# Kernel tuning notes

Hardware: AMD Instinct MI355X
Metric: run time of the kernel (lower is better)

The kernel has to match this reference:

```python
import jax, jax.numpy as jnp
import numpy as np

N, E = 100000, 1600000
IN_C, HID, OUT_C, EDGE_D, GRAPH_D = 32, 32, 8, 16, 16

def _lin_w(key, fan_in, fan_out):
    return jax.random.normal(key, (fan_in, fan_out), dtype=jnp.float32) * (1.0 / np.sqrt(fan_in))

def setup_inputs() -> dict:
    key = jax.random.key(0)
    ks = jax.random.split(key, 12)
    return {
        "x": jax.random.uniform(ks[0], (N, IN_C), dtype=jnp.float32),
        "edge_attr": jax.random.uniform(ks[1], (E, EDGE_D), dtype=jnp.float32),
        "graph_attr": jax.random.uniform(ks[2], (1, GRAPH_D), dtype=jnp.float32),
        "edge_index": jax.random.randint(ks[3], (2, E), 0, N, dtype=jnp.int32),
        "batch": jnp.zeros((N,), dtype=jnp.int32),
        "W_node": _lin_w(ks[4], IN_C, HID),
        "b_node": jnp.zeros((HID,), jnp.float32),
        "W_graph": _lin_w(ks[5], GRAPH_D, GRAPH_D),
        "b_graph": jnp.zeros((GRAPH_D,), jnp.float32),
        "W_edge_agg": _lin_w(ks[6], 2 * HID + EDGE_D + GRAPH_D, EDGE_D),
        "b_edge_agg": jnp.zeros((EDGE_D,), jnp.float32),
        "W_node_agg": _lin_w(ks[7], EDGE_D + HID + GRAPH_D, HID),
        "b_node_agg": jnp.zeros((HID,), jnp.float32),
        "W_sage_l": _lin_w(ks[8], HID, OUT_C),
        "b_sage_l": jnp.zeros((OUT_C,), jnp.float32),
        "W_sage_r": _lin_w(ks[9], HID, OUT_C),
    }

def _seg_mean(vals, idx, num_segments):
    # scatter-mean: sum per segment / count (count clamped to 1 for empty segments)
    sums = jax.ops.segment_sum(vals, idx, num_segments=num_segments)
    cnt = jax.ops.segment_sum(jnp.ones((vals.shape[0],), vals.dtype), idx, num_segments=num_segments)
    return sums / jnp.maximum(cnt, 1.0)[:, None]

def reference(x, edge_attr, graph_attr, edge_index, batch,
              W_node, b_node, W_graph, b_graph,
              W_edge_agg, b_edge_agg, W_node_agg, b_node_agg,
              W_sage_l, b_sage_l, W_sage_r):
    n = x.shape[0]
    row, col = edge_index[0], edge_index[1]
    # node / graph embeddings (plain linear, no activation)
    h_i = x @ W_node + b_node                       # [N, HID]
    h_G = graph_attr @ W_graph + b_graph            # [1, GRAPH_D]
    h_G_e = jnp.broadcast_to(h_G, (row.shape[0], h_G.shape[1]))
    # edge aggregator: gather both endpoints, concat, linear, relu
    edge_in = jnp.concatenate([h_i[row], h_i[col], edge_attr, h_G_e], axis=-1)  # [E, 96]
    h_edge_agg = jax.nn.relu(edge_in @ W_edge_agg + b_edge_agg)                 # [E, EDGE_D]
    # per-node mean of edges whose source == node (replaces O(N*E) python loop)
    m_N = _seg_mean(h_edge_agg, row, n)             # [N, EDGE_D]
    # node aggregator
    h_G_n = jnp.broadcast_to(h_G, (n, h_G.shape[1]))
    h_i2 = jax.nn.relu(jnp.concatenate([h_i, m_N, h_G_n], axis=-1) @ W_node_agg + b_node_agg)
    # SAGEConv (mean aggr): out = lin_l(mean_{j->i} x_j) + lin_r(x_i)
    agg = _seg_mean(h_i2[row], col, n)
    h_nodes = agg @ W_sage_l + b_sage_l + h_i2 @ W_sage_r  # [N, OUT_C]
    # global mean pool over batch assignment (single graph here)
    pooled = _seg_mean(h_nodes, batch, 1)           # [1, OUT_C]
    return jax.nn.log_softmax(pooled, axis=1)
```

## Files before the change

kernel.cpp:

```cpp
#include <hip/hip_runtime.h>
#include <hip/hip_fp16.h>

#define HID 32
#define IN_C 32
#define EDGE_D 16
#define GRAPH_D 16
#define OUT_C 8
#define STRIDE 48

__global__ void __launch_bounds__(256)
k_node_emb(const float* __restrict__ x,
           const float* __restrict__ W,
           const float* __restrict__ b,
           const float* __restrict__ graph_attr,
           const float* __restrict__ W_graph,
           const float* __restrict__ b_graph,
           const float* __restrict__ W_edge_agg,
           const float* __restrict__ b_edge_agg,
           const float* __restrict__ W_node_agg,
           const float* __restrict__ b_node_agg,
           float* __restrict__ bias_edge,
           float* __restrict__ bias_node,
           int* __restrict__ zero_base, int zero_count,
           __half* __restrict__ h, int n) {
    __shared__ float hG[GRAPH_D];
    int t = threadIdx.x;
    for (int idx = blockIdx.x * blockDim.x + t; idx < zero_count;
         idx += gridDim.x * blockDim.x)
        zero_base[idx] = 0;

    if (blockIdx.x == 0 && t < GRAPH_D) {
        float acc = b_graph[t];
        for (int d = 0; d < GRAPH_D; d++)
            acc += graph_attr[d] * W_graph[d * GRAPH_D + t];
        hG[t] = acc;
    }
    __syncthreads();
    if (blockIdx.x == 0) {
        if (t < EDGE_D) {
            float acc = b_edge_agg[t];
            for (int d = 0; d < GRAPH_D; d++)
                acc += hG[d] * W_edge_agg[(2 * HID + EDGE_D + d) * EDGE_D + t];
            bias_edge[t] = acc;
        }
        if (t < HID) {
            float acc = b_node_agg[t];
            for (int d = 0; d < GRAPH_D; d++)
                acc += hG[d] * W_node_agg[(HID + EDGE_D + d) * HID + t];
            bias_node[t] = acc;
        }
    }

    int i = blockIdx.x * blockDim.x + t;
    if (i >= n) return;
    float in[IN_C];
    const float4* xr = (const float4*)(x + (size_t)i * IN_C);
#pragma unroll
    for (int q = 0; q < IN_C / 4; q++) {
        float4 v = xr[q];
        in[4 * q + 0] = v.x; in[4 * q + 1] = v.y;
        in[4 * q + 2] = v.z; in[4 * q + 3] = v.w;
    }
    float acc[HID];
#pragma unroll
    for (int j = 0; j < HID; j++) acc[j] = b[j];
#pragma unroll
    for (int k = 0; k < IN_C; k++) {
        float a = in[k];
#pragma unroll
        for (int j = 0; j < HID; j++) acc[j] += a * W[k * HID + j];
    }
    float4 packed[4];
    __half2* ph = (__half2*)packed;
#pragma unroll
    for (int j = 0; j < 16; j++)
        ph[j] = __floats2half2_rn(acc[2 * j], acc[2 * j + 1]);
    float4* hr = (float4*)(h + (size_t)i * HID);
#pragma unroll
    for (int q = 0; q < 4; q++) hr[q] = packed[q];
}

__global__ void __launch_bounds__(256)
k_edge_place(const int* __restrict__ ei,
             const __half* __restrict__ hi,
             const float* __restrict__ ea,
             const float* __restrict__ We,
             const float* __restrict__ biasE,
             int* __restrict__ cur_row,
             int* __restrict__ cur_col,
             __half* __restrict__ he_bucket, int E) {
    int e = blockIdx.x * blockDim.x + threadIdx.x;
    if (e >= E) return;
    int r = ei[e];
    int c = ei[E + e];
    int pr = atomicAdd(cur_row + r, 1);
    atomicAdd(cur_col + c, 1);

    float in[80];
    {
        float4 t[4];
        const float4* hr4 = (const float4*)(hi + (size_t)r * HID);
#pragma unroll
        for (int q = 0; q < 4; q++) t[q] = hr4[q];
        const __half2* hp = (const __half2*)t;
#pragma unroll
        for (int j = 0; j < 16; j++) {
            float2 f = __half22float2(hp[j]);
            in[2 * j] = f.x; in[2 * j + 1] = f.y;
        }
    }
    {
        float4 t[4];
        const float4* hc4 = (const float4*)(hi + (size_t)c * HID);
#pragma unroll
        for (int q = 0; q < 4; q++) t[q] = hc4[q];
        const __half2* hp = (const __half2*)t;
#pragma unroll
        for (int j = 0; j < 16; j++) {
            float2 f = __half22float2(hp[j]);
            in[32 + 2 * j] = f.x; in[32 + 2 * j + 1] = f.y;
        }
    }
    {
        const float4* er = (const float4*)(ea + (size_t)e * EDGE_D);
#pragma unroll
        for (int q = 0; q < 4; q++) {
            float4 v = er[q];
            in[64 + 4 * q + 0] = v.x; in[64 + 4 * q + 1] = v.y;
            in[64 + 4 * q + 2] = v.z; in[64 + 4 * q + 3] = v.w;
        }
    }
    float acc[EDGE_D];
#pragma unroll
    for (int j = 0; j < EDGE_D; j++) acc[j] = biasE[j];
#pragma unroll
    for (int k = 0; k < 80; k++) {
        float a = in[k];
#pragma unroll
        for (int j = 0; j < EDGE_D; j++) acc[j] += a * We[k * EDGE_D + j];
    }

    if (pr < STRIDE) {
        float4 packed[2];
        __half2* ph = (__half2*)packed;
#pragma unroll
        for (int j = 0; j < 8; j++)
            ph[j] = __floats2half2_rn(fmaxf(acc[2 * j], 0.f),
                                      fmaxf(acc[2 * j + 1], 0.f));
        float4* dst = (float4*)(he_bucket + ((size_t)r * STRIDE + pr) * EDGE_D);
        dst[0] = packed[0];
        dst[1] = packed[1];
    }
}

#define RNODES 128
__global__ void __launch_bounds__(256)
k_reduce(const __half* __restrict__ hi,
         const __half* __restrict__ he_bucket,
         const int* __restrict__ cur_row,
         const int* __restrict__ batch,
         const float* __restrict__ Wna,
         const float* __restrict__ Wsl,
         const float* __restrict__ Wsr,
         const float* __restrict__ biasN,
         __half* __restrict__ zout,
         float* __restrict__ pool,
         float* __restrict__ ncnt, int n) {
    __shared__ float ms_s[RNODES][EDGE_D + 1];
    __shared__ int cnt_s[RNODES];
    __shared__ float red[4][OUT_C + 1];
    __shared__ float redc[4];
    int tid = threadIdx.x;
    int g = tid >> 4;
    int l = tid & 15;
    int base = blockIdx.x * RNODES;

    if (tid < RNODES)
        cnt_s[tid] = (base + tid < n) ? cur_row[base + tid] : 0;
    __syncthreads();

    for (int iter = 0; iter < RNODES / 16; iter++) {
        int node = base + iter * 16 + g;
        int cnt = cnt_s[iter * 16 + g];
        int d = cnt < STRIDE ? cnt : STRIDE;
        float inv = 1.0f / fmaxf((float)cnt, 1.0f);
        float a16[EDGE_D];
#pragma unroll
        for (int j = 0; j < EDGE_D; j++) a16[j] = 0.f;
        const __half* bb = he_bucket + (size_t)node * STRIDE * EDGE_D;
        for (int t = l; t < d; t += 16) {
            const float4* rp = (const float4*)(bb + t * EDGE_D);
            float4 lo = rp[0], hi4 = rp[1];
            const __half2* hp0 = (const __half2*)&lo;
            const __half2* hp1 = (const __half2*)&hi4;
#pragma unroll
            for (int j = 0; j < 4; j++) {
                float2 f0 = __half22float2(hp0[j]);
                float2 f1 = __half22float2(hp1[j]);
                a16[2 * j]     += f0.x; a16[2 * j + 1] += f0.y;
                a16[8 + 2 * j] += f1.x; a16[8 + 2 * j + 1] += f1.y;
            }
        }
#pragma unroll
        for (int m = 8; m >= 1; m >>= 1) {
#pragma unroll
            for (int k = 0; k < m; k++) {
                float send = (l & m) ? a16[k] : a16[k + m];
                float recv = __shfl_xor(send, m, 16);
                float keep = (l & m) ? a16[k + m] : a16[k];
                a16[k] = keep + recv;
            }
        }
        ms_s[iter * 16 + g][l] = a16[0] * inv;
    }
    __syncthreads();

    int i = base + tid;
    float rvv[OUT_C];
#pragma unroll
    for (int j = 0; j < OUT_C; j++) rvv[j] = 0.f;
    float cc = 0.f;

    if (tid < RNODES && i < n) {
        float ms[EDGE_D];
#pragma unroll
        for (int k = 0; k < EDGE_D; k++) ms[k] = ms_s[tid][k];

        float hr[HID];
        {
            float4 t[4];
            const float4* hrow = (const float4*)(hi + (size_t)i * HID);
#pragma unroll
            for (int q = 0; q < 4; q++) t[q] = hrow[q];
            const __half2* hp = (const __half2*)t;
#pragma unroll
            for (int j = 0; j < 16; j++) {
                float2 f = __half22float2(hp[j]);
                hr[2 * j] = f.x; hr[2 * j + 1] = f.y;
            }
        }
        float h2[HID];
#pragma unroll
        for (int j = 0; j < HID; j++) h2[j] = biasN[j];
#pragma unroll
        for (int k = 0; k < HID; k++) {
            float a = hr[k];
#pragma unroll
            for (int j = 0; j < HID; j++) h2[j] += a * Wna[k * HID + j];
        }
#pragma unroll
        for (int k = 0; k < EDGE_D; k++) {
            float a = ms[k];
#pragma unroll
            for (int j = 0; j < HID; j++) h2[j] += a * Wna[(HID + k) * HID + j];
        }
#pragma unroll
        for (int j = 0; j < HID; j++) h2[j] = fmaxf(h2[j], 0.f);

        float zv[OUT_C];
#pragma unroll
        for (int j = 0; j < OUT_C; j++) zv[j] = 0.f;
#pragma unroll
        for (int k = 0; k < HID; k++) {
            float a = h2[k];
#pragma unroll
            for (int j = 0; j < OUT_C; j++) {
                zv[j]  += a * Wsl[k * OUT_C + j];
                rvv[j] += a * Wsr[k * OUT_C + j];
            }
        }
        float4 packed;
        __half2* ph = (__half2*)&packed;
#pragma unroll
        for (int j = 0; j < 4; j++)
            ph[j] = __floats2half2_rn(zv[2 * j], zv[2 * j + 1]);
        *(float4*)(zout + (size_t)i * OUT_C) = packed;
        if (batch[i] == 0) cc = 1.f; else {
#pragma unroll
            for (int j = 0; j < OUT_C; j++) rvv[j] = 0.f;
        }
    }
#pragma unroll
    for (int off = 32; off > 0; off >>= 1) {
#pragma unroll
        for (int j = 0; j < OUT_C; j++) rvv[j] += __shfl_down(rvv[j], off, 64);
        cc += __shfl_down(cc, off, 64);
    }
    int w = tid >> 6;
    if ((tid & 63) == 0) {
#pragma unroll
        for (int j = 0; j < OUT_C; j++) red[w][j] = rvv[j];
        redc[w] = cc;
    }
    __syncthreads();
    if (tid < OUT_C) {
        float s = red[0][tid] + red[1][tid] + red[2][tid] + red[3][tid];
        atomicAdd(pool + tid, s);
    }
    if (tid == OUT_C) {
        atomicAdd(ncnt, redc[0] + redc[1] + redc[2] + redc[3]);
    }
}

#define POOL_BLOCKS 1280
__global__ void __launch_bounds__(256)
k_pool(const int* __restrict__ ei,
       const __half* __restrict__ z,
       const int* __restrict__ cur_col,
       float* __restrict__ pool, int E) {
    __shared__ float red[4][OUT_C + 1];
    int tid = threadIdx.x;
    float w8[OUT_C];
#pragma unroll
    for (int j = 0; j < OUT_C; j++) w8[j] = 0.f;
    for (int e = blockIdx.x * blockDim.x + tid; e < E;
         e += gridDim.x * blockDim.x) {
        int r = ei[e];
        int c = ei[E + e];
        float inv = 1.0f / fmaxf((float)cur_col[c], 1.0f);
        float4 t = *(const float4*)(z + (size_t)r * OUT_C);
        const __half2* hp = (const __half2*)&t;
#pragma unroll
        for (int j = 0; j < 4; j++) {
            float2 f = __half22float2(hp[j]);
            w8[2 * j]     += f.x * inv;
            w8[2 * j + 1] += f.y * inv;
        }
    }
#pragma unroll
    for (int off = 32; off > 0; off >>= 1) {
#pragma unroll
        for (int j = 0; j < OUT_C; j++) w8[j] += __shfl_down(w8[j], off, 64);
    }
    int w = tid >> 6;
    if ((tid & 63) == 0) {
#pragma unroll
        for (int j = 0; j < OUT_C; j++) red[w][j] = w8[j];
    }
    __syncthreads();
    if (tid < OUT_C) {
        float s = red[0][tid] + red[1][tid] + red[2][tid] + red[3][tid];
        atomicAdd(pool + tid, s);
    }
}

__global__ void k_final(const float* __restrict__ pool,
                        const float* __restrict__ ncnt,
                        const float* __restrict__ bsl,
                        float* __restrict__ out) {
    if (threadIdx.x == 0 && blockIdx.x == 0) {
        float c = fmaxf(ncnt[0], 1.0f);
        float p[OUT_C];
        float m = -1e30f;
#pragma unroll
        for (int j = 0; j < OUT_C; j++) {
            p[j] = pool[j] / c + bsl[j];
            m = fmaxf(m, p[j]);
        }
        float s = 0.f;
#pragma unroll
        for (int j = 0; j < OUT_C; j++) s += expf(p[j] - m);
        float l = logf(s);
#pragma unroll
        for (int j = 0; j < OUT_C; j++) out[j] = p[j] - m - l;
    }
}

extern "C" void kernel_launch(void* const* d_in, const int* in_sizes, int n_in,
                              void* d_out, int out_size, void* d_ws, size_t ws_size,
                              hipStream_t stream) {
    const float* x          = (const float*)d_in[0];
    const float* edge_attr  = (const float*)d_in[1];
    const float* graph_attr = (const float*)d_in[2];
    const int*   edge_index = (const int*)d_in[3];
    const int*   batch      = (const int*)d_in[4];
    const float* W_node     = (const float*)d_in[5];
    const float* b_node     = (const float*)d_in[6];
    const float* W_graph    = (const float*)d_in[7];
    const float* b_graph    = (const float*)d_in[8];
    const float* W_edge_agg = (const float*)d_in[9];
    const float* b_edge_agg = (const float*)d_in[10];
    const float* W_node_agg = (const float*)d_in[11];
    const float* b_node_agg = (const float*)d_in[12];
    const float* W_sage_l   = (const float*)d_in[13];
    const float* b_sage_l   = (const float*)d_in[14];
    const float* W_sage_r   = (const float*)d_in[15];

    const int n = in_sizes[0] / IN_C;
    const int E = in_sizes[3] / 2;

    char* wsb = (char*)d_ws;
    int*  cur_row = (int*)wsb;
    int*  cur_col = cur_row + n;
    float* pool   = (float*)(cur_col + n);
    float* ncnt   = pool + 8;
    int   zero_count = 2 * n + 16;
    size_t off = (size_t)zero_count * 4;
    __half* he_bucket = (__half*)(wsb + off); off += (size_t)n * STRIDE * EDGE_D * 2;
    __half* h_i  = (__half*)(wsb + off); off += (size_t)n * HID * 2;
    __half* zarr = (__half*)(wsb + off); off += (size_t)n * OUT_C * 2;
    float* biasE = (float*)(wsb + off);  off += 16 * 4;
    float* biasN = (float*)(wsb + off);

    k_node_emb<<<(n + 255) / 256, 256, 0, stream>>>(x, W_node, b_node,
                                                    graph_attr, W_graph, b_graph,
                                                    W_edge_agg, b_edge_agg,
                                                    W_node_agg, b_node_agg,
                                                    biasE, biasN,
                                                    cur_row, zero_count, h_i, n);

    k_edge_place<<<(E + 255) / 256, 256, 0, stream>>>(edge_index, h_i, edge_attr,
                                                      W_edge_agg, biasE,
                                                      cur_row, cur_col,
                                                      he_bucket, E);

    k_reduce<<<(n + RNODES - 1) / RNODES, 256, 0, stream>>>(h_i, he_bucket, cur_row,
                                                            batch, W_node_agg,
                                                            W_sage_l, W_sage_r,
                                                            biasN, zarr, pool, ncnt, n);

    k_pool<<<POOL_BLOCKS, 256, 0, stream>>>(edge_index, zarr, cur_col, pool, E);

    k_final<<<1, 64, 0, stream>>>(pool, ncnt, b_sage_l, (float*)d_out);
}
```

Before: 507.8 us.

## Precompute per-node edge-linear projections to shrink per-edge gather and matmul

```diff
diff --git a/kernel.cpp b/kernel.cpp
--- a/kernel.cpp
+++ b/kernel.cpp
@@ -22,7 +22,9 @@
            float* __restrict__ bias_edge,
            float* __restrict__ bias_node,
            int* __restrict__ zero_base, int zero_count,
-           __half* __restrict__ h, int n) {
+           __half* __restrict__ h,
+           __half* __restrict__ Pr,
+           __half* __restrict__ Pc, int n) {
     __shared__ float hG[GRAPH_D];
     int t = threadIdx.x;
     for (int idx = blockIdx.x * blockDim.x + t; idx < zero_count;
@@ -78,11 +80,39 @@
     float4* hr = (float4*)(h + (size_t)i * HID);
 #pragma unroll
     for (int q = 0; q < 4; q++) hr[q] = packed[q];
+
+    float pr[EDGE_D], pc[EDGE_D];
+#pragma unroll
+    for (int j = 0; j < EDGE_D; j++) { pr[j] = 0.f; pc[j] = 0.f; }
+#pragma unroll
+    for (int k = 0; k < HID; k++) {
+        float a = acc[k];
+#pragma unroll
+        for (int j = 0; j < EDGE_D; j++) {
+            pr[j] += a * W_edge_agg[k * EDGE_D + j];
+            pc[j] += a * W_edge_agg[(HID + k) * EDGE_D + j];
+        }
+    }
+    float4 pk[2];
+    __half2* pp = (__half2*)pk;
+#pragma unroll
+    for (int j = 0; j < 8; j++) pp[j] = __floats2half2_rn(pr[2 * j], pr[2 * j + 1]);
+    {
+        float4* d0 = (float4*)(Pr + (size_t)i * EDGE_D);
+        d0[0] = pk[0]; d0[1] = pk[1];
+    }
+#pragma unroll
+    for (int j = 0; j < 8; j++) pp[j] = __floats2half2_rn(pc[2 * j], pc[2 * j + 1]);
+    {
+        float4* d1 = (float4*)(Pc + (size_t)i * EDGE_D);
+        d1[0] = pk[0]; d1[1] = pk[1];
+    }
 }
 
 __global__ void __launch_bounds__(256)
 k_edge_place(const int* __restrict__ ei,
-             const __half* __restrict__ hi,
+             const __half* __restrict__ Pr,
+             const __half* __restrict__ Pc,
              const float* __restrict__ ea,
              const float* __restrict__ We,
              const float* __restrict__ biasE,
@@ -96,48 +126,45 @@
     int pr = atomicAdd(cur_row + r, 1);
     atomicAdd(cur_col + c, 1);
 
-    float in[80];
-    {
-        float4 t[4];
-        const float4* hr4 = (const float4*)(hi + (size_t)r * HID);
-#pragma unroll
-        for (int q = 0; q < 4; q++) t[q] = hr4[q];
-        const __half2* hp = (const __half2*)t;
-#pragma unroll
-        for (int j = 0; j < 16; j++) {
-            float2 f = __half22float2(hp[j]);
-            in[2 * j] = f.x; in[2 * j + 1] = f.y;
-        }
-    }
-    {
-        float4 t[4];
-        const float4* hc4 = (const float4*)(hi + (size_t)c * HID);
-#pragma unroll
-        for (int q = 0; q < 4; q++) t[q] = hc4[q];
-        const __half2* hp = (const __half2*)t;
-#pragma unroll
-        for (int j = 0; j < 16; j++) {
-            float2 f = __half22float2(hp[j]);
-            in[32 + 2 * j] = f.x; in[32 + 2 * j + 1] = f.y;
-        }
-    }
+    const float4* prp = (const float4*)(Pr + (size_t)r * EDGE_D);
+    const float4* pcp = (const float4*)(Pc + (size_t)c * EDGE_D);
+    float4 g0 = prp[0], g1 = prp[1];
+    float4 q0 = pcp[0], q1 = pcp[1];
+    float eav[EDGE_D];
     {
         const float4* er = (const float4*)(ea + (size_t)e * EDGE_D);
 #pragma unroll
         for (int q = 0; q < 4; q++) {
             float4 v = er[q];
-            in[64 + 4 * q + 0] = v.x; in[64 + 4 * q + 1] = v.y;
-            in[64 + 4 * q + 2] = v.z; in[64 + 4 * q + 3] = v.w;
-        }
-    }
+            eav[4 * q + 0] = v.x; eav[4 * q + 1] = v.y;
+            eav[4 * q + 2] = v.z; eav[4 * q + 3] = v.w;
+        }
+    }
+
     float acc[EDGE_D];
-#pragma unroll
-    for (int j = 0; j < EDGE_D; j++) acc[j] = biasE[j];
-#pragma unroll
-    for (int k = 0; k < 80; k++) {
-        float a = in[k];
-#pragma unroll
-        for (int j = 0; j < EDGE_D; j++) acc[j] += a * We[k * EDGE_D + j];
+    {
+        const __half2* h0 = (const __half2*)&g0;
+        const __half2* h1 = (const __half2*)&g1;
+        const __half2* k0 = (const __half2*)&q0;
+        const __half2* k1 = (const __half2*)&q1;
+#pragma unroll
+        for (int j = 0; j < 4; j++) {
+            float2 a0 = __half22float2(h0[j]);
+            float2 b0 = __half22float2(k0[j]);
+            acc[2 * j]     = biasE[2 * j]     + a0.x + b0.x;
+            acc[2 * j + 1] = biasE[2 * j + 1] + a0.y + b0.y;
+            float2 a1 = __half22float2(h1[j]);
+            float2 b1 = __half22float2(k1[j]);
+            acc[8 + 2 * j]     = biasE[8 + 2 * j]     + a1.x + b1.x;
+            acc[8 + 2 * j + 1] = biasE[8 + 2 * j + 1] + a1.y + b1.y;
+        }
+    }
+#pragma unroll
+    for (int k = 0; k < EDGE_D; k++) {
+        float a = eav[k];
+#pragma unroll
+        for (int j = 0; j < EDGE_D; j++)
+            acc[j] += a * We[(2 * HID + k) * EDGE_D + j];
     }
 
     if (pr < STRIDE) {
@@ -400,16 +427,19 @@
     __half* h_i  = (__half*)(wsb + off); off += (size_t)n * HID * 2;
     __half* zarr = (__half*)(wsb + off); off += (size_t)n * OUT_C * 2;
     float* biasE = (float*)(wsb + off);  off += 16 * 4;
-    float* biasN = (float*)(wsb + off);
+    float* biasN = (float*)(wsb + off);  off += HID * 4;
+    __half* Pr = (__half*)(wsb + off);   off += (size_t)n * EDGE_D * 2;
+    __half* Pc = (__half*)(wsb + off);   off += (size_t)n * EDGE_D * 2;
 
     k_node_emb<<<(n + 255) / 256, 256, 0, stream>>>(x, W_node, b_node,
                                                     graph_attr, W_graph, b_graph,
                                                     W_edge_agg, b_edge_agg,
                                                     W_node_agg, b_node_agg,
                                                     biasE, biasN,
-                                                    cur_row, zero_count, h_i, n);
-
-    k_edge_place<<<(E + 255) / 256, 256, 0, stream>>>(edge_index, h_i, edge_attr,
+                                                    cur_row, zero_count, h_i,
+                                                    Pr, Pc, n);
+
+    k_edge_place<<<(E + 255) / 256, 256, 0, stream>>>(edge_index, Pr, Pc, edge_attr,
                                                       W_edge_agg, biasE,
                                                       cur_row, cur_col,
                                                       he_bucket, E);
```

Measured after the change: 466.7 us. 8.1% less time.
